# Kernel tuning notes

Hardware: AMD Instinct MI355X
Metric: run time of the kernel (lower is better)

The kernel has to match this reference:

```python
import jax, jax.numpy as jnp
import numpy as np

B, C, N = 8, 256, 2048
NMOD = 5  # time, space, time_cor, space_cor, global_res


def _attn(x, y, Wqk, Vw, Vb, Tw, Tb):
    """Offset self-attention (PCT-style). x, y: [B, C, N].
    q/k share the same 1x1-conv weight Wqk; v and trans convs have bias.
    softmax over last axis, then L1 renorm over axis=1 of the [B,N,N] map.
    """
    x_q = jnp.einsum('oc,bcn->bno', Wqk, y)           # [B,N,C]
    x_k = jnp.einsum('oc,bcn->bon', Wqk, x)           # [B,C,N]
    x_v = jnp.einsum('oc,bcn->bon', Vw, x) + Vb[:, None]
    att = jax.nn.softmax(jnp.einsum('bnc,bcm->bnm', x_q, x_k), axis=-1)
    att = att / (1e-07 + att.sum(axis=1, keepdims=True))
    x_r = jnp.einsum('bcn,bnm->bcm', x_v, att)        # [B,C,N]
    x_r = jax.nn.relu(jnp.einsum('oc,bcn->bon', Tw, x - x_r) + Tb[:, None])
    return x + x_r


def setup_inputs() -> dict:
    key = jax.random.key(0)
    ks = jax.random.split(key, 6)
    s = 1.0 / np.sqrt(C)
    return {
        'x':   jax.random.normal(ks[0], (B, 3, C, N), dtype=jnp.float32),
        'Wqk': jax.random.normal(ks[1], (NMOD, C, C), dtype=jnp.float32) * s,
        'Vw':  jax.random.normal(ks[2], (NMOD, C, C), dtype=jnp.float32) * s,
        'Vb':  jax.random.normal(ks[3], (NMOD, C), dtype=jnp.float32) * s,
        'Tw':  jax.random.normal(ks[4], (NMOD, C, C), dtype=jnp.float32) * s,
        'Tb':  jax.random.normal(ks[5], (NMOD, C), dtype=jnp.float32) * s,
    }


def reference(x, Wqk, Vw, Vb, Tw, Tb):
    time_x, mid, space_x = x[:, 0], x[:, 1], x[:, 2]

    def A(i, xx, yy):
        return _attn(xx, yy, Wqk[i], Vw[i], Vb[i], Tw[i], Tb[i])

    time_att = A(0, time_x, time_x)
    space_att = A(1, space_x, space_x)
    time_cor = A(2, time_x, space_x)
    space_cor = A(3, space_x, time_x)
    global_feat = A(4, mid, mid)

    time_update = jnp.tanh(time_att * jax.nn.sigmoid(time_cor))
    space_update = jnp.tanh(space_att * jax.nn.sigmoid(space_cor))
    g_sig = jax.nn.sigmoid(global_feat)
    global_residual = jax.nn.sigmoid(time_update * g_sig + space_update * g_sig)
    return mid + global_residual * jnp.tanh(global_feat)
```

## Files before the change

### kernel.cpp

```cpp
#include <hip/hip_runtime.h>
#include <math.h>

#define BB 8
#define CC 256
#define NN 2048

static const size_t NC  = (size_t)NN * CC;
static const size_t CN  = (size_t)CC * NN;

typedef unsigned short u16;
typedef __attribute__((ext_vector_type(8))) short short8;
typedef __attribute__((ext_vector_type(4))) float f32x4;

__device__ __forceinline__ float bf2f(u16 v) {
    union { unsigned int u; float f; } t; t.u = ((unsigned int)v) << 16; return t.f;
}
__device__ __forceinline__ u16 f2bf(float f) {
    union { float f; unsigned int u; } t; t.f = f;
    return (u16)((t.u + 0x7fffu + ((t.u >> 16) & 1u)) >> 16);
}
__device__ __forceinline__ float sigf(float x) { return 1.0f / (1.0f + expf(-x)); }

__device__ __forceinline__ size_t til(int r, int c, int tpr) {
    return (((size_t)((r >> 4) * tpr + (c >> 5))) << 9)
         + (size_t)((r & 15) << 5) + (size_t)(c & 31);
}

__global__ __launch_bounds__(256) void cast_w(const float* __restrict__ in,
                                              u16* __restrict__ outp)
{
    const int mat = blockIdx.y;
    const int idx = blockIdx.x * 256 + threadIdx.x;
    const int c = idx >> 6, k = (idx & 63) << 2;
    const float4 v = *(const float4*)&in[(size_t)mat * (CC * CC) + (size_t)c * CC + k];
    ushort4 p;
    p.x = f2bf(v.x); p.y = f2bf(v.y); p.z = f2bf(v.z); p.w = f2bf(v.w);
    *(ushort4*)&outp[(size_t)mat * (CC * CC) + til(c, k, CC / 32)] = p;
}

__global__ __launch_bounds__(256) void tcast_x(const float* __restrict__ in,
                                               u16* __restrict__ out)
{
    const int z = blockIdx.z;
    const float* I = in + (size_t)z * CN;
    u16* O = out + (size_t)z * NC;
    const int c0 = blockIdx.y * 64, n0 = blockIdx.x * 64;
    const int tx = threadIdx.x & 15, ty = threadIdx.x >> 4;

    __shared__ float t[64][68];

    #pragma unroll
    for (int cc = 0; cc < 64; cc += 16) {
        const int c = ty + cc;
        *(float4*)&t[c][tx * 4] = *(const float4*)&I[(size_t)(c0 + c) * NN + n0 + tx * 4];
    }
    __syncthreads();
    #pragma unroll
    for (int nn2 = 0; nn2 < 64; nn2 += 16) {
        const int n = n0 + ty + nn2;
        const int c = c0 + tx * 4;
        ushort4 p;
        p.x = f2bf(t[tx * 4 + 0][ty + nn2]);
        p.y = f2bf(t[tx * 4 + 1][ty + nn2]);
        p.z = f2bf(t[tx * 4 + 2][ty + nn2]);
        p.w = f2bf(t[tx * 4 + 3][ty + nn2]);
        *(ushort4*)&O[til(n, c, 8)] = p;
    }
}

struct QkvP {
    const u16* w[12]; const u16* x[12]; u16* out[12];
    const float* bias[12]; int isv[12];
};

__global__ __launch_bounds__(256) void conv_qkv(QkvP P)
{
    const int z = blockIdx.z, job = z >> 3, b = z & 7;
    const int isv = P.isv[job];
    const u16* Wp = P.w[job];
    const u16* Xp = P.x[job] + (size_t)b * (3 * NC);
    const int n0 = blockIdx.x * 128, c0 = blockIdx.y * 128;
    const int lane = threadIdx.x & 63, wave = threadIdx.x >> 6;
    const int l15 = lane & 15, lg = lane >> 4;
    const int rA = (wave >> 1) * 64, rB = (wave & 1) * 64;

    const u16* Ab = isv ? Xp : Wp;
    const u16* Bb = isv ? Wp : Xp;
    const int Ar0 = (isv ? n0 : c0) + rA;
    const int Br0 = (isv ? c0 : n0) + rB;

    const u16* ap[4]; const u16* bp[4];
    #pragma unroll
    for (int i = 0; i < 4; i++) {
        ap[i] = Ab + til(Ar0 + i * 16 + l15, lg * 8, 8);
        bp[i] = Bb + til(Br0 + i * 16 + l15, lg * 8, 8);
    }

    f32x4 acc[4][4] = {};
    #pragma unroll 2
    for (int kc = 0; kc < 8; kc++) {
        short8 av[4], bv[4];
        #pragma unroll
        for (int i = 0; i < 4; i++) av[i] = *(const short8*)(ap[i] + kc * 512);
        #pragma unroll
        for (int i = 0; i < 4; i++) bv[i] = *(const short8*)(bp[i] + kc * 512);
        #pragma unroll
        for (int i = 0; i < 4; i++)
            #pragma unroll
            for (int j = 0; j < 4; j++)
                acc[i][j] = __builtin_amdgcn_mfma_f32_16x16x32_bf16(av[i], bv[j], acc[i][j], 0, 0, 0);
    }

    if (!isv) {
        u16* Ot = P.out[job] + (size_t)b * NC;
        #pragma unroll
        for (int i = 0; i < 4; i++) {
            const int c = c0 + rA + i * 16 + lg * 4;
            #pragma unroll
            for (int j = 0; j < 4; j++) {
                const int n = n0 + rB + j * 16 + l15;
                ushort4 p;
                p.x = f2bf(acc[i][j][0]); p.y = f2bf(acc[i][j][1]);
                p.z = f2bf(acc[i][j][2]); p.w = f2bf(acc[i][j][3]);
                *(ushort4*)&Ot[til(n, c, 8)] = p;
            }
        }
    } else {
        u16* Ov = P.out[job] + (size_t)b * CN;
        const float* bias = P.bias[job];
        #pragma unroll
        for (int j = 0; j < 4; j++) {
            const int c = c0 + rB + j * 16 + l15;
            const float bi = bias[c];
            #pragma unroll
            for (int i = 0; i < 4; i++) {
                const int n = n0 + rA + i * 16 + lg * 4;
                ushort4 p;
                p.x = f2bf(acc[i][j][0] + bi); p.y = f2bf(acc[i][j][1] + bi);
                p.z = f2bf(acc[i][j][2] + bi); p.w = f2bf(acc[i][j][3] + bi);
                *(ushort4*)&Ov[til(c, n, 64)] = p;
            }
        }
    }
}

__global__ __launch_bounds__(256) void conv_t2(
    const u16* __restrict__ W, const u16* __restrict__ Dt,
    const float* __restrict__ bias, const u16* __restrict__ Xts,
    u16* __restrict__ O)
{
    const int bid = blockIdx.x;
    const int b = bid & 7;
    const int rest = bid >> 3;
    const int cy = rest & 1, nx = rest >> 1;
    const int n0 = nx * 128, c0 = cy * 128;
    const int lane = threadIdx.x & 63, wave = threadIdx.x >> 6;
    const int l15 = lane & 15, lg = lane >> 4;
    const int wc = (wave >> 1) * 64, wn = (wave & 1) * 64;

    const u16* Xp = Dt + (size_t)b * NC;
    const u16* ap[4]; const u16* bp[4];
    #pragma unroll
    for (int i = 0; i < 4; i++) {
        ap[i] = W  + til(c0 + wc + i * 16 + l15, lg * 8, 8);
        bp[i] = Xp + til(n0 + wn + i * 16 + l15, lg * 8, 8);
    }

    f32x4 acc[4][4] = {};
    #pragma unroll 2
    for (int kc = 0; kc < 8; kc++) {
        short8 av[4], bv[4];
        #pragma unroll
        for (int i = 0; i < 4; i++) av[i] = *(const short8*)(ap[i] + kc * 512);
        #pragma unroll
        for (int i = 0; i < 4; i++) bv[i] = *(const short8*)(bp[i] + kc * 512);
        #pragma unroll
        for (int i = 0; i < 4; i++)
            #pragma unroll
            for (int j = 0; j < 4; j++)
                acc[i][j] = __builtin_amdgcn_mfma_f32_16x16x32_bf16(av[i], bv[j], acc[i][j], 0, 0, 0);
    }

    const u16* Xtb = Xts + (size_t)b * (3 * NC);
    u16* Ob = O + (size_t)b * CN;
    #pragma unroll
    for (int i = 0; i < 4; i++) {
        const int cb = c0 + wc + i * 16 + lg * 4;
        #pragma unroll
        for (int j = 0; j < 4; j++) {
            const int n = n0 + wn + j * 16 + l15;
            const ushort4 xv = *(const ushort4*)&Xtb[til(n, cb, 8)];
            const u16 xa[4] = { xv.x, xv.y, xv.z, xv.w };
            #pragma unroll
            for (int r = 0; r < 4; r++) {
                const int c = cb + r;
                const float v = bf2f(xa[r]) + fmaxf(acc[i][j][r] + bias[c], 0.0f);
                Ob[til(c, n, 64)] = f2bf(v);
            }
        }
    }
}

__global__ __launch_bounds__(1024) void attn_mfma4(
    const u16* __restrict__ Q, const u16* __restrict__ K,
    u16* __restrict__ Sout, float* __restrict__ CPb)
{
    const int bid = blockIdx.x;
    const int b = bid & 7;
    const int nblk = bid >> 3;
    const int n0 = nblk * 32;
    const int tid = threadIdx.x, lane = tid & 63, wave = tid >> 6;
    const int l15 = lane & 15, lg = lane >> 4;

    const u16* Qt = Q + (size_t)b * NC;
    const u16* Kt = K + (size_t)b * NC;

    f32x4 acc[2][8];
    #pragma unroll
    for (int g = 0; g < 2; g++)
        #pragma unroll
        for (int t = 0; t < 8; t++) acc[g][t] = (f32x4){0.f, 0.f, 0.f, 0.f};

    const u16* qb0 = Qt + til(n0 + l15,      lg * 8, 8);
    const u16* qb1 = Qt + til(n0 + 16 + l15, lg * 8, 8);
    const u16* kb  = Kt + til(wave * 128 + l15, lg * 8, 8);

    #pragma unroll
    for (int kc = 0; kc < 8; kc++) {
        const short8 a0 = *(const short8*)(qb0 + kc * 512);
        const short8 a1 = *(const short8*)(qb1 + kc * 512);
        short8 bf[8];
        #pragma unroll
        for (int t = 0; t < 8; t++)
            bf[t] = *(const short8*)(kb + t * 4096 + kc * 512);
        #pragma unroll
        for (int t = 0; t < 8; t++) {
            acc[0][t] = __builtin_amdgcn_mfma_f32_16x16x32_bf16(a0, bf[t], acc[0][t], 0, 0, 0);
            acc[1][t] = __builtin_amdgcn_mfma_f32_16x16x32_bf16(a1, bf[t], acc[1][t], 0, 0, 0);
        }
    }

    __shared__ float red[16][32];
    __shared__ float rowstat[32];

    float pm[2][4];
    #pragma unroll
    for (int g = 0; g < 2; g++)
        #pragma unroll
        for (int r = 0; r < 4; r++) {
            float m = acc[g][0][r];
            #pragma unroll
            for (int t = 1; t < 8; t++) m = fmaxf(m, acc[g][t][r]);
            #pragma unroll
            for (int o = 1; o <= 8; o <<= 1) m = fmaxf(m, __shfl_xor(m, o));
            pm[g][r] = m;
        }
    if (l15 == 0) {
        #pragma unroll
        for (int g = 0; g < 2; g++)
            #pragma unroll
            for (int r = 0; r < 4; r++) red[wave][g * 16 + lg * 4 + r] = pm[g][r];
    }
    __syncthreads();
    if (tid < 32) {
        float m = red[0][tid];
        #pragma unroll
        for (int w = 1; w < 16; w++) m = fmaxf(m, red[w][tid]);
        rowstat[tid] = m;
    }
    __syncthreads();

    float rm[2][4], ps[2][4];
    #pragma unroll
    for (int g = 0; g < 2; g++)
        #pragma unroll
        for (int r = 0; r < 4; r++) { rm[g][r] = rowstat[g * 16 + lg * 4 + r]; ps[g][r] = 0.f; }
    __syncthreads();

    #pragma unroll
    for (int g = 0; g < 2; g++)
        #pragma unroll
        for (int t = 0; t < 8; t++)
            #pragma unroll
            for (int r = 0; r < 4; r++) {
                const float e = __expf(acc[g][t][r] - rm[g][r]);
                acc[g][t][r] = e; ps[g][r] += e;
            }
    #pragma unroll
    for (int g = 0; g < 2; g++)
        #pragma unroll
        for (int r = 0; r < 4; r++)
            #pragma unroll
            for (int o = 1; o <= 8; o <<= 1) ps[g][r] += __shfl_xor(ps[g][r], o);
    if (l15 == 0) {
        #pragma unroll
        for (int g = 0; g < 2; g++)
            #pragma unroll
            for (int r = 0; r < 4; r++) red[wave][g * 16 + lg * 4 + r] = ps[g][r];
    }
    __syncthreads();
    if (tid < 32) {
        float s = red[0][tid];
        #pragma unroll
        for (int w = 1; w < 16; w++) s += red[w][tid];
        rowstat[tid] = 1.0f / s;
    }
    __syncthreads();

    float rv[2][4];
    #pragma unroll
    for (int g = 0; g < 2; g++)
        #pragma unroll
        for (int r = 0; r < 4; r++) rv[g][r] = rowstat[g * 16 + lg * 4 + r];

    u16* sb = Sout + (size_t)b * NN * NN;
    u16* sbg[2];
    #pragma unroll
    for (int g = 0; g < 2; g++)
        sbg[g] = sb + (size_t)((n0 >> 3) + g * 2 + (lg >> 1)) * (NN * 8) + (lg & 1) * 4;
    float* cpb = CPb + ((size_t)b * 64 + nblk) * NN;

    #pragma unroll
    for (int t = 0; t < 8; t++) {
        const int m = wave * 128 + t * 16 + l15;
        float cs = 0.0f;
        #pragma unroll
        for (int g = 0; g < 2; g++) {
            const float v0 = acc[g][t][0] * rv[g][0], v1 = acc[g][t][1] * rv[g][1];
            const float v2 = acc[g][t][2] * rv[g][2], v3 = acc[g][t][3] * rv[g][3];
            ushort4 pk;
            pk.x = f2bf(v0); pk.y = f2bf(v1); pk.z = f2bf(v2); pk.w = f2bf(v3);
            *(ushort4*)&sbg[g][(size_t)m * 8] = pk;
            cs += v0 + v1 + v2 + v3;
        }
        cs += __shfl_xor(cs, 16);
        cs += __shfl_xor(cs, 32);
        if (lane < 16) cpb[m] = cs;
    }
}

__global__ __launch_bounds__(256) void csum_kernel(const float* __restrict__ cp,
                                                   float* __restrict__ cs)
{
    const int b  = blockIdx.y;
    const int ml = threadIdx.x & 63;
    const int m  = blockIdx.x * 64 + ml;
    const int g0 = threadIdx.x >> 6;
    float s = 0.0f;
    for (int g = g0; g < 64; g += 4)
        s += cp[((size_t)b * 64 + g) * NN + m];
    __shared__ float red[4][64];
    red[g0][ml] = s;
    __syncthreads();
    if (threadIdx.x < 64) {
        cs[(size_t)b * NN + blockIdx.x * 64 + threadIdx.x] =
            red[0][threadIdx.x] + red[1][threadIdx.x] +
            red[2][threadIdx.x] + red[3][threadIdx.x];
    }
}

__global__ __launch_bounds__(256) void pv_mfma(
    const u16* __restrict__ V, const u16* __restrict__ S,
    const float* __restrict__ CSb, const u16* __restrict__ Xts,
    u16* __restrict__ DTo)
{
    const int bid = blockIdx.x;
    const int b = bid & 7;
    const int r2 = bid >> 3;
    const int cy = r2 & 1, mx = r2 >> 1;
    const int m0b = mx * 64, c0 = cy * 128;
    const int lane = threadIdx.x & 63, wave = threadIdx.x >> 6;
    const int wc = (wave >> 1) * 64, wm = (wave & 1) * 32;
    const int l15 = lane & 15, lg = lane >> 4;

    const u16* Vm = V + (size_t)b * CN;
    const u16* Sm = S + (size_t)b * NN * NN;

    f32x4 acc[4][2] = {};
    const u16* vp[4]; const u16* sp[2];
    #pragma unroll
    for (int ai = 0; ai < 4; ai++)
        vp[ai] = Vm + til(c0 + wc + ai * 16 + l15, lg * 8, 64);
    #pragma unroll
    for (int bj = 0; bj < 2; bj++)
        sp[bj] = Sm + ((size_t)lg * NN + m0b + wm + bj * 16 + l15) * 8;

    #pragma unroll 2
    for (int kc = 0; kc < 64; kc++) {
        short8 a[4], s2[2];
        #pragma unroll
        for (int ai = 0; ai < 4; ai++) { a[ai] = *(const short8*)vp[ai]; vp[ai] += 512; }
        #pragma unroll
        for (int bj = 0; bj < 2; bj++) { s2[bj] = *(const short8*)sp[bj]; sp[bj] += (size_t)4 * NN * 8; }
        #pragma unroll
        for (int ai = 0; ai < 4; ai++)
            #pragma unroll
            for (int bj = 0; bj < 2; bj++)
                acc[ai][bj] = __builtin_amdgcn_mfma_f32_16x16x32_bf16(a[ai], s2[bj], acc[ai][bj], 0, 0, 0);
    }

    const u16* Xtb = Xts + (size_t)b * (3 * NC);
    u16* Dtb = DTo + (size_t)b * NC;

    #pragma unroll
    for (int bj = 0; bj < 2; bj++) {
        const int m = m0b + wm + bj * 16 + l15;
        const float inv = 1.0f / (1e-7f + CSb[(size_t)b * NN + m]);
        #pragma unroll
        for (int ai = 0; ai < 4; ai++) {
            const int c = c0 + wc + ai * 16 + lg * 4;
            const size_t ad = til(m, c, 8);
            const ushort4 xv = *(const ushort4*)&Xtb[ad];
            ushort4 pk;
            pk.x = f2bf(bf2f(xv.x) - acc[ai][bj][0] * inv);
            pk.y = f2bf(bf2f(xv.y) - acc[ai][bj][1] * inv);
            pk.z = f2bf(bf2f(xv.z) - acc[ai][bj][2] * inv);
            pk.w = f2bf(bf2f(xv.w) - acc[ai][bj][3] * inv);
            *(ushort4*)&Dtb[ad] = pk;
        }
    }
}

__global__ __launch_bounds__(256) void ew_update_t(u16* __restrict__ A,
                                                   const u16* __restrict__ Bv)
{
    const size_t e = ((size_t)blockIdx.x * 256 + threadIdx.x) * 8;
    short8 a = *(const short8*)&A[e];
    const short8 b = *(const short8*)&Bv[e];
    #pragma unroll
    for (int j = 0; j < 8; j++) {
        const float f = tanhf(bf2f((u16)a[j]) * sigf(bf2f((u16)b[j])));
        a[j] = (short)f2bf(f);
    }
    *(short8*)&A[e] = a;
}

__global__ __launch_bounds__(256) void ew_final_t(
    const u16* __restrict__ TU, const u16* __restrict__ SU,
    const u16* __restrict__ G, const float* __restrict__ x,
    float* __restrict__ OUT)
{
    const size_t e = ((size_t)blockIdx.x * 256 + threadIdx.x) * 8;
    const int b = (int)(e / CN);
    const size_t r = e - (size_t)b * CN;
    const int tile = (int)(r >> 9), win = (int)(r & 511);
    const int row = win >> 5, col = win & 31;
    const int c = (tile >> 6) * 16 + row;
    const int n = (tile & 63) * 32 + col;

    const size_t lin = ((size_t)b * 3 + 1) * CN + (size_t)c * NN + n;
    const float4 m0 = *(const float4*)&x[lin];
    const float4 m1 = *(const float4*)&x[lin + 4];
    const float mid[8] = { m0.x, m0.y, m0.z, m0.w, m1.x, m1.y, m1.z, m1.w };

    const short8 tu = *(const short8*)&TU[e];
    const short8 su = *(const short8*)&SU[e];
    const short8 g  = *(const short8*)&G[e];

    float o[8];
    #pragma unroll
    for (int j = 0; j < 8; j++) {
        const float gg = bf2f((u16)g[j]);
        o[j] = mid[j] + sigf((bf2f((u16)tu[j]) + bf2f((u16)su[j])) * sigf(gg)) * tanhf(gg);
    }
    float* op = OUT + (size_t)b * CN + (size_t)c * NN + n;
    *(float4*)op       = (float4){o[0], o[1], o[2], o[3]};
    *(float4*)(op + 4) = (float4){o[4], o[5], o[6], o[7]};
}

extern "C" void kernel_launch(void* const* d_in, const int* in_sizes, int n_in,
                              void* d_out, int out_size, void* d_ws, size_t ws_size,
                              hipStream_t stream)
{
    const float* x   = (const float*)d_in[0];
    const float* Wqk = (const float*)d_in[1];
    const float* Vw  = (const float*)d_in[2];
    const float* VbF = (const float*)d_in[3];
    const float* Tw  = (const float*)d_in[4];
    const float* TbF = (const float*)d_in[5];
    float* out = (float*)d_out;

    const int mxs[5] = {0, 2, 0, 2, 1};
    const int mys[5] = {0, 2, 2, 0, 1};
    const int qjob[5] = {0, 1, 5, 6, 4};
    const int q_wi[7] = {0, 1, 2, 3, 4, 2, 3};
    const int q_xi[7] = {0, 2, 0, 2, 1, 2, 0};

    const size_t WSZ     = (size_t)CC * CC;
    const size_t QK_SLAB = (size_t)BB * NC;
    const size_t S_SLAB  = (size_t)BB * NN * NN;
    const size_t CP_SLAB = (size_t)BB * 64 * NN;
    const size_t CS_SLAB = (size_t)BB * NN;
    const size_t O_SLAB  = (size_t)BB * CN;

    const size_t base_b = 15 * WSZ * 2 + (size_t)BB * 3 * NC * 2;
    const size_t modtl  = S_SLAB * 2 + CP_SLAB * 4 + CS_SLAB * 4 + QK_SLAB * 2;
    const size_t margin = 2u << 20;
    const size_t need_1 = base_b + 12 * QK_SLAB * 2 + modtl + 3 * O_SLAB * 2 + margin;
    const size_t need_2 = base_b +  3 * QK_SLAB * 2 + modtl + 3 * O_SLAB * 2 + margin;

    const int tier2 = (ws_size >= need_1) ? 0 : 1;
    if (tier2 && ws_size < need_2) return;

    const int nQK = tier2 ? 2 : 7;
    const int nV  = tier2 ? 1 : 5;

    char* ws = (char*)d_ws;
    size_t off = 0;
    auto alloc = [&](size_t bytes) -> char* {
        char* p = ws + off; off += (bytes + 255) & ~255ULL; return p;
    };

    u16*   W16 = (u16*)  alloc(15 * WSZ * 2);
    u16*   Xt  = (u16*)  alloc((size_t)BB * 3 * NC * 2);
    u16*   QK  = (u16*)  alloc((size_t)nQK * QK_SLAB * 2);
    u16*   VB  = (u16*)  alloc((size_t)nV * QK_SLAB * 2);
    u16*   S   = (u16*)  alloc(S_SLAB * 2);
    float* CP  = (float*)alloc(CP_SLAB * 4);
    float* CS  = (float*)alloc(CS_SLAB * 4);
    u16*   DT  = (u16*)  alloc(QK_SLAB * 2);
    u16*   OB  = (u16*)  alloc(3 * O_SLAB * 2);

    cast_w<<<dim3(64, 5), 256, 0, stream>>>(Wqk, W16);
    cast_w<<<dim3(64, 5), 256, 0, stream>>>(Vw,  W16 + 5 * WSZ);
    cast_w<<<dim3(64, 5), 256, 0, stream>>>(Tw,  W16 + 10 * WSZ);
    tcast_x<<<dim3(NN / 64, CC / 64, BB * 3), 256, 0, stream>>>(x, Xt);

    if (!tier2) {
        QkvP qp{};
        for (int j = 0; j < 7; j++) {
            qp.w[j] = W16 + (size_t)q_wi[j] * WSZ;
            qp.x[j] = Xt + (size_t)q_xi[j] * NC;
            qp.out[j] = QK + (size_t)j * QK_SLAB;
            qp.isv[j] = 0; qp.bias[j] = nullptr;
        }
        for (int i = 0; i < 5; i++) {
            const int j = 7 + i;
            qp.w[j] = W16 + (size_t)(5 + i) * WSZ;
            qp.x[j] = Xt + (size_t)mxs[i] * NC;
            qp.out[j] = VB + (size_t)i * QK_SLAB;
            qp.isv[j] = 1; qp.bias[j] = VbF + (size_t)i * CC;
        }
        conv_qkv<<<dim3(NN / 128, CC / 128, 96), 256, 0, stream>>>(qp);
    }

    auto run_mod = [&](int i, u16* O) {
        const u16* Qp; const u16* Kp; const u16* Vp;
        if (!tier2) {
            Qp = QK + (size_t)qjob[i] * QK_SLAB;
            Kp = QK + (size_t)i * QK_SLAB;
            Vp = VB + (size_t)i * QK_SLAB;
        } else {
            QkvP qp{}; int nj = 0;
            qp.w[nj] = W16 + (size_t)i * WSZ; qp.x[nj] = Xt + (size_t)mxs[i] * NC;
            qp.out[nj] = QK; qp.isv[nj] = 0; nj++;
            Qp = QK; Kp = QK;
            if (mys[i] != mxs[i]) {
                qp.w[nj] = W16 + (size_t)i * WSZ; qp.x[nj] = Xt + (size_t)mys[i] * NC;
                qp.out[nj] = QK + QK_SLAB; qp.isv[nj] = 0; nj++;
                Qp = QK + QK_SLAB;
            }
            qp.w[nj] = W16 + (size_t)(5 + i) * WSZ; qp.x[nj] = Xt + (size_t)mxs[i] * NC;
            qp.out[nj] = VB; qp.isv[nj] = 1; qp.bias[nj] = VbF + (size_t)i * CC; nj++;
            conv_qkv<<<dim3(NN / 128, CC / 128, 8 * nj), 256, 0, stream>>>(qp);
            Vp = VB;
        }
        attn_mfma4<<<512, 1024, 0, stream>>>(Qp, Kp, S, CP);
        csum_kernel<<<dim3(NN / 64, BB), 256, 0, stream>>>(CP, CS);
        pv_mfma<<<512, 256, 0, stream>>>(Vp, S, CS, Xt + (size_t)mxs[i] * NC, DT);
        conv_t2<<<256, 256, 0, stream>>>(W16 + (size_t)(10 + i) * WSZ, DT,
                                         TbF + (size_t)i * CC,
                                         Xt + (size_t)mxs[i] * NC, O);
    };

    u16* OB0 = OB;
    u16* OB1 = OB + O_SLAB;
    u16* OB2 = OB + 2 * O_SLAB;
    const int ewg = (int)(((size_t)BB * CN) / (256 * 8));

    run_mod(0, OB0);
    run_mod(2, OB1);
    ew_update_t<<<ewg, 256, 0, stream>>>(OB0, OB1);
    run_mod(1, OB1);
    run_mod(3, OB2);
    ew_update_t<<<ewg, 256, 0, stream>>>(OB1, OB2);
    run_mod(4, OB2);
    ew_final_t<<<ewg, 256, 0, stream>>>(OB0, OB1, OB2, x, out);
}
```

Measured before the change: 709.8 us.

## Stage Q/K tiles through LDS with async global_load_lds prefetch ring

The QK^T score kernel now stages the Q tiles and a ring of eight K tile slots per wave in shared memory using asynchronous global-to-LDS loads. K loads are issued six tiles ahead, with vmcnt waits gating each MFMA pair, so load latency can overlap matrix math instead of loading all operands into registers up front. MFMA issue is also wrapped in raised wave priority. The cost is about 144KB of LDS per block and more fragile hand-written wait-count and ordering logic.

```diff
diff --git a/kernel.cpp b/kernel.cpp
--- a/kernel.cpp
+++ b/kernel.cpp
@@ -25,6 +25,14 @@
     return (((size_t)((r >> 4) * tpr + (c >> 5))) << 9)
          + (size_t)((r & 15) << 5) + (size_t)(c & 31);
 }
+
+__device__ __forceinline__ void stage_tile(const u16* gtile, u16* ldst, int lane) {
+    const u16* src = gtile + (lane & 15) * 32 + (lane >> 4) * 8;
+    __builtin_amdgcn_global_load_lds(
+        (const __attribute__((address_space(1))) void*)src,
+        (__attribute__((address_space(3))) void*)ldst, 16, 0, 0);
+}
+#define WAITV(n) asm volatile("s_waitcnt vmcnt(" #n ")" ::: "memory")
 
 __global__ __launch_bounds__(256) void cast_w(const float* __restrict__ in,
                                               u16* __restrict__ outp)
@@ -201,7 +209,7 @@
     }
 }
 
-__global__ __launch_bounds__(1024) void attn_mfma4(
+__global__ __launch_bounds__(1024) void attn_mfma6(
     const u16* __restrict__ Q, const u16* __restrict__ K,
     u16* __restrict__ Sout, float* __restrict__ CPb)
 {
@@ -215,33 +223,48 @@
     const u16* Qt = Q + (size_t)b * NC;
     const u16* Kt = K + (size_t)b * NC;
 
-    f32x4 acc[2][8];
-    #pragma unroll
-    for (int g = 0; g < 2; g++)
-        #pragma unroll
-        for (int t = 0; t < 8; t++) acc[g][t] = (f32x4){0.f, 0.f, 0.f, 0.f};
-
-    const u16* qb0 = Qt + til(n0 + l15,      lg * 8, 8);
-    const u16* qb1 = Qt + til(n0 + 16 + l15, lg * 8, 8);
-    const u16* kb  = Kt + til(wave * 128 + l15, lg * 8, 8);
-
-    #pragma unroll
-    for (int kc = 0; kc < 8; kc++) {
-        const short8 a0 = *(const short8*)(qb0 + kc * 512);
-        const short8 a1 = *(const short8*)(qb1 + kc * 512);
-        short8 bf[8];
-        #pragma unroll
-        for (int t = 0; t < 8; t++)
-            bf[t] = *(const short8*)(kb + t * 4096 + kc * 512);
-        #pragma unroll
-        for (int t = 0; t < 8; t++) {
-            acc[0][t] = __builtin_amdgcn_mfma_f32_16x16x32_bf16(a0, bf[t], acc[0][t], 0, 0, 0);
-            acc[1][t] = __builtin_amdgcn_mfma_f32_16x16x32_bf16(a1, bf[t], acc[1][t], 0, 0, 0);
-        }
-    }
-
+    __shared__ u16 KL[16 * 8 * 512];
+    __shared__ u16 QL[16 * 512];
     __shared__ float red[16][32];
     __shared__ float rowstat[32];
+
+    stage_tile(Qt + ((size_t)((n0 >> 4) + (wave >> 3)) * 8 + (wave & 7)) * 512,
+               &QL[wave * 512], lane);
+    u16* kw = &KL[wave * 4096];
+    #pragma unroll
+    for (int p = 0; p < 6; p++)
+        stage_tile(Kt + ((size_t)(wave * 8 + (p & 7)) * 8 + (p >> 3)) * 512,
+                   &kw[p * 512], lane);
+    __syncthreads();
+
+    f32x4 acc[2][8];
+    #pragma unroll
+    for (int g = 0; g < 2; g++)
+        #pragma unroll
+        for (int t = 0; t < 8; t++) acc[g][t] = (f32x4){0.f, 0.f, 0.f, 0.f};
+
+    const int roff = lg * 128 + l15 * 8;
+
+    #pragma unroll
+    for (int kc = 0; kc < 8; kc++) {
+        const short8 a0 = *(const short8*)&QL[kc * 512 + roff];
+        const short8 a1 = *(const short8*)&QL[(8 + kc) * 512 + roff];
+        #pragma unroll
+        for (int t = 0; t < 8; t++) {
+            const int i = kc * 8 + t;
+            if (i < 58) { WAITV(5); } else if (i == 58) { WAITV(0); }
+            const short8 bf = *(const short8*)&kw[(i & 7) * 512 + roff];
+            if (i + 6 < 64) {
+                const int j = i + 6;
+                stage_tile(Kt + ((size_t)(wave * 8 + (j & 7)) * 8 + (j >> 3)) * 512,
+                           &kw[(j & 7) * 512], lane);
+            }
+            __builtin_amdgcn_s_setprio(1);
+            acc[0][t] = __builtin_amdgcn_mfma_f32_16x16x32_bf16(a0, bf, acc[0][t], 0, 0, 0);
+            acc[1][t] = __builtin_amdgcn_mfma_f32_16x16x32_bf16(a1, bf, acc[1][t], 0, 0, 0);
+            __builtin_amdgcn_s_setprio(0);
+        }
+    }
 
     float pm[2][4];
     #pragma unroll
@@ -565,7 +588,7 @@
             conv_qkv<<<dim3(NN / 128, CC / 128, 8 * nj), 256, 0, stream>>>(qp);
             Vp = VB;
         }
-        attn_mfma4<<<512, 1024, 0, stream>>>(Qp, Kp, S, CP);
+        attn_mfma6<<<512, 1024, 0, stream>>>(Qp, Kp, S, CP);
         csum_kernel<<<dim3(NN / 64, BB), 256, 0, stream>>>(CP, CS);
         pv_mfma<<<512, 256, 0, stream>>>(Vp, S, CS, Xt + (size_t)mxs[i] * NC, DT);
         conv_t2<<<256, 256, 0, stream>>>(W16 + (size_t)(10 + i) * WSZ, DT,
```

Result: faster. 648.6 us (-8.6%).
